# Optimization experiments

Hardware: AMD Instinct MI355X
Metric: run time of the kernel (lower is better)

Reference implementation:

```python
import jax, jax.numpy as jnp
import numpy as np

D_MODEL = 128
K_RED = 3          # fd_redundancy_k
MAX_ITERS = 16     # upper bound on the data-dependent while-loop; masked no-ops after convergence
NEG = -1e9


def setup_inputs() -> dict:
    key = jax.random.key(0)
    ks = jax.random.split(key, 10)
    B, U, S, D, F = 16, 2048, 512, D_MODEL, 32
    return {
        "user_enc": jax.random.normal(ks[0], (B, U, D), jnp.float32),
        "server_enc": jax.random.normal(ks[1], (B, S, D), jnp.float32),
        "users": jax.random.uniform(ks[2], (B, U, 6), jnp.float32),
        "servers": jax.random.uniform(ks[3], (B, S, 7), jnp.float32),
        "connect": jax.random.randint(ks[4], (B, U, S), 0, 2, jnp.int32),
        "fd_onehot": jax.random.randint(ks[5], (B, S, F), 0, 2, jnp.int32),
        "state_proj_w": jax.random.normal(ks[6], (D, 4), jnp.float32) * 0.05,
        "state_proj_b": jnp.zeros((D,), jnp.float32),
        "fd_bias": jnp.asarray(1.0, jnp.float32),
        "ptr_q_w": jax.random.normal(ks[7], (D, D), jnp.float32) * (D ** -0.5),
        "ptr_k_w": jax.random.normal(ks[8], (D, D), jnp.float32) * (D ** -0.5),
        "user_state_w": jax.random.normal(ks[9], (1, 3), jnp.float32) * 0.05,
        "score_bias": jnp.zeros((1,), jnp.float32),
    }


def _forward(user_enc, server_enc, users, servers, connect, fd_onehot,
             state_proj_w, state_proj_b, fd_bias, ptr_q_w, ptr_k_w,
             user_state_w, score_bias):
    B, U, _ = users.shape
    S = servers.shape[1]
    D = user_enc.shape[-1]
    needs = users[..., 2:6]                    # [B,U,4]
    init_cap = servers[..., 3:7]               # [B,S,4]
    connect_mask = connect.astype(bool)
    fd = fd_onehot.astype(jnp.float32)         # [B,S,F] in {0,1}
    F = fd.shape[-1]
    inv_sqrt_d = D ** -0.5
    tk = jnp.float32(max(K_RED, 1))
    q = user_enc @ ptr_q_w.T                   # [B,U,D]  (loop-invariant)
    u_ids = jnp.arange(U)
    s_ids = jnp.arange(S)

    def body(carry, _):
        alloc, cap, seen, logp, flag = carry
        replica_count = alloc.sum(-1)                                    # [B,U]
        need_more = replica_count < K_RED
        can_fulfill = jnp.all(cap[:, None] >= needs[:, :, None], axis=-1)  # [B,U,S]
        eligible = connect_mask & can_fulfill & need_more[..., None] & ~alloc
        go = flag & jnp.any(need_more) & jnp.any(eligible)

        # pointer-attention logits with dynamic server state
        is_new_fd = (jnp.einsum('buf,bsf->bus', seen, fd) < 0.5).astype(jnp.float32)
        cap_ratio = cap / jnp.maximum(init_cap, 1e-6)
        k_vec = (server_enc + cap_ratio @ state_proj_w.T + state_proj_b) @ ptr_k_w.T
        logits = jnp.einsum('bud,bsd->bus', q, k_vec) * inv_sqrt_d + score_bias
        logits = logits + fd_bias * is_new_fd
        rc = replica_count.astype(jnp.float32)
        user_state = jnp.stack([rc / tk,
                                jnp.clip(K_RED - rc, 0.0, None) / tk,
                                (replica_count == K_RED - 1).astype(jnp.float32)], axis=-1)
        logits = logits + user_state @ user_state_w.T                    # broadcast [B,U,1]

        cand = jnp.where(eligible, logits, NEG)
        # each valid server greedily proposes its best eligible user
        valid_server = jnp.any(eligible, axis=1)                         # [B,S]
        prop_u = jnp.argmax(cand, axis=1)                                # [B,S]
        prop_mask = valid_server[:, None, :] & (u_ids[None, :, None] == prop_u[:, None, :])
        logp_prop = jnp.max(cand, axis=1) - jax.nn.logsumexp(cand, axis=1)  # [B,S]

        # each proposed user accepts the highest-scoring proposing server
        acc_cand = jnp.where(prop_mask, logits, NEG)
        has_prop = jnp.any(prop_mask, axis=2)                            # [B,U]
        chosen_s = jnp.argmax(acc_cand, axis=2)                          # [B,U]
        accepted = has_prop[..., None] & (s_ids == chosen_s[..., None])  # [B,U,S]

        alloc = alloc | (accepted & go)
        fd_gain = (jnp.einsum('bus,bsf->buf', prop_mask.astype(jnp.float32), fd) > 0).astype(jnp.float32)
        seen = jnp.where(go, jnp.maximum(seen, fd_gain), seen)
        used = jnp.einsum('bus,buc->bsc', accepted.astype(jnp.float32), needs)
        cap = jnp.where(go, jnp.maximum(cap - used, 0.0), cap)
        gathered = jnp.take_along_axis(logp_prop, chosen_s, axis=1)      # [B,U]
        logp = logp + jnp.where(go & has_prop, gathered, 0.0)
        return (alloc, cap, seen, logp, go), None

    init = (jnp.zeros((B, U, S), bool), init_cap,
            jnp.zeros((B, U, F), jnp.float32), jnp.zeros((B, U), jnp.float32),
            jnp.asarray(True))
    (alloc, cap, seen, logp, _), _ = jax.lax.scan(body, init, None, length=MAX_ITERS)
    return logp.sum(axis=1), alloc, cap


def reference(user_enc, server_enc, users, servers, connect, fd_onehot,
              state_proj_w, state_proj_b, fd_bias, ptr_q_w, ptr_k_w,
              user_state_w, score_bias):
    # policy='greedy' branch of the original forward
    return _forward(user_enc, server_enc, users, servers, connect, fd_onehot,
                    state_proj_w, state_proj_b, fd_bias, ptr_q_w, ptr_k_w,
                    user_state_w, score_bias)
```

## Files before the change

### kernel.cpp

```cpp
#include <hip/hip_runtime.h>
#include <hip/hip_bf16.h>

#define B_N 16
#define U_N 2048
#define S_N 512
#define D_N 128
#define INV_SQRT_D 0.08838834764831845f

typedef unsigned long long ull;
typedef __attribute__((ext_vector_type(8))) short bf16x8;
typedef __attribute__((ext_vector_type(4))) float f32x4;
typedef __attribute__((ext_vector_type(4))) _Float16 f16x4;

__device__ __forceinline__ unsigned monof(float v) {
    unsigned b = __float_as_uint(v);
    return (b & 0x80000000u) ? ~b : (b | 0x80000000u);
}
__device__ __forceinline__ float unmonof(unsigned m) {
    unsigned b = (m & 0x80000000u) ? (m & 0x7fffffffu) : ~m;
    return __uint_as_float(b);
}
__device__ __forceinline__ unsigned short f2bf(float x) {
    unsigned u = __float_as_uint(x);
    return (unsigned short)((u + 0x7fffu + ((u >> 16) & 1u)) >> 16);
}

__global__ void init_pack(const float* __restrict__ servers, const float* __restrict__ users,
                          const int* __restrict__ fd_onehot, const int* __restrict__ connect,
                          ull* __restrict__ connU,
                          unsigned* allocU, uint4* alloc3, unsigned* rcArr, unsigned* seenArr,
                          float* logp, float* capA, float* invA, unsigned* fdm, float* nds,
                          unsigned* any_valid, int* aCnt, int* aList) {
    {
        int r = blockIdx.x * 4 + (threadIdx.x >> 6);
        int lane = threadIdx.x & 63;
        const int* row = connect + (size_t)r * S_N;
        #pragma unroll
        for (int c = 0; c < 8; ++c) {
            ull m = __ballot(row[c * 64 + lane] != 0);
            if (lane == 0) connU[(size_t)r * 8 + c] = m;
        }
    }
    int i = blockIdx.x * 256 + threadIdx.x;
    if (i < B_N * U_N * 16) allocU[i] = 0u;
    if (i < B_N * U_N) {
        rcArr[i] = 0u; seenArr[i] = 0u; logp[i] = 0.f;
        alloc3[i] = make_uint4(0xFFFFFFFFu, 0xFFFFFFFFu, 0xFFFFFFFFu, 0xFFFFFFFFu);
        aList[i] = i & 2047;
        const float* up = users + (size_t)i * 6;
        nds[i * 4 + 0] = up[2]; nds[i * 4 + 1] = up[3];
        nds[i * 4 + 2] = up[4]; nds[i * 4 + 3] = up[5];
    }
    if (i < B_N * S_N) {
        const float* sp = servers + (size_t)i * 7;
        float4 c = make_float4(sp[3], sp[4], sp[5], sp[6]);
        ((float4*)capA)[i] = c;
        ((float4*)invA)[i] = make_float4(1.f / fmaxf(c.x, 1e-6f), 1.f / fmaxf(c.y, 1e-6f),
                                         1.f / fmaxf(c.z, 1e-6f), 1.f / fmaxf(c.w, 1e-6f));
        unsigned w = 0u;
        const int* fp = fd_onehot + (size_t)i * 32;
        #pragma unroll
        for (int f = 0; f < 32; ++f) w |= (fp[f] != 0 ? 1u : 0u) << f;
        fdm[i] = w;
    }
    if (i < 32) aCnt[i] = (i < 16) ? (int)U_N : 0;
    if (i < 16) any_valid[i] = 0u;
}

__global__ __launch_bounds__(256) void gemm_both(const float* __restrict__ user_enc,
                                                 const float* __restrict__ server_enc,
                                                 const float* __restrict__ spb,
                                                 const float* __restrict__ qw,
                                                 const float* __restrict__ kw,
                                                 float* __restrict__ q,
                                                 unsigned short* __restrict__ qb,
                                                 unsigned short* __restrict__ kb) {
    __shared__ float As[16][68];
    __shared__ float Bs[16][68];
    const int z = blockIdx.z;
    const bool isK = blockIdx.x < 8;
    const int xb = isK ? blockIdx.x : blockIdx.x - 8;
    const int M = isK ? S_N : U_N;
    const float* Ab = (isK ? server_enc : user_enc) + (size_t)z * M * D_N;
    const float* Bb = isK ? kw : qw;
    const float scale = isK ? INV_SQRT_D : 1.0f;
    const int m0 = xb * 64, n0 = blockIdx.y * 64;
    const int tid = threadIdx.x;
    const int tx = tid & 15, ty = tid >> 4;
    const int lrow = tid >> 2, lk = (tid & 3) * 4;
    float acc[4][4] = {};
    for (int k0 = 0; k0 < D_N; k0 += 16) {
        float4 av = *(const float4*)(Ab + (size_t)(m0 + lrow) * D_N + k0 + lk);
        float4 bv = *(const float4*)(Bb + (size_t)(n0 + lrow) * D_N + k0 + lk);
        if (isK) {
            const float4 sv = *(const float4*)(spb + k0 + lk);
            av.x += sv.x; av.y += sv.y; av.z += sv.z; av.w += sv.w;
        }
        __syncthreads();
        As[lk + 0][lrow] = av.x; As[lk + 1][lrow] = av.y; As[lk + 2][lrow] = av.z; As[lk + 3][lrow] = av.w;
        Bs[lk + 0][lrow] = bv.x; Bs[lk + 1][lrow] = bv.y; Bs[lk + 2][lrow] = bv.z; Bs[lk + 3][lrow] = bv.w;
        __syncthreads();
        #pragma unroll
        for (int kk = 0; kk < 16; ++kk) {
            float4 a = *(const float4*)&As[kk][ty * 4];
            float4 bq = *(const float4*)&Bs[kk][tx * 4];
            float ar[4] = {a.x, a.y, a.z, a.w}, br[4] = {bq.x, bq.y, bq.z, bq.w};
            #pragma unroll
            for (int ii = 0; ii < 4; ++ii)
                #pragma unroll
                for (int jj = 0; jj < 4; ++jj) acc[ii][jj] += ar[ii] * br[jj];
        }
    }
    #pragma unroll
    for (int ii = 0; ii < 4; ++ii) {
        float4 o = make_float4(acc[ii][0] * scale, acc[ii][1] * scale,
                               acc[ii][2] * scale, acc[ii][3] * scale);
        size_t idx = (size_t)z * M * D_N + (size_t)(m0 + ty * 4 + ii) * D_N + n0 + tx * 4;
        ushort4 ob;
        ob.x = f2bf(o.x); ob.y = f2bf(o.y); ob.z = f2bf(o.z); ob.w = f2bf(o.w);
        if (isK) {
            *(ushort4*)(kb + idx) = ob;
        } else {
            *(float4*)(q + idx) = o;
            *(ushort4*)(qb + idx) = ob;
        }
    }
}

__global__ void qm_kernel(const float* __restrict__ q, const float* __restrict__ kw,
                          const float* __restrict__ spw, float* __restrict__ qm) {
    __shared__ float qs[64][129];
    __shared__ float m2s[512];
    __shared__ float sps[512];
    int b = blockIdx.y, u0 = blockIdx.x * 64;
    int t = threadIdx.x;
    for (int i = t; i < 512; i += 256) sps[i] = spw[i];
    #pragma unroll
    for (int it = 0; it < 8; ++it) {
        int f4 = t + 256 * it;
        int row = f4 >> 5;
        int col = (f4 & 31) * 4;
        float4 v = *(const float4*)(q + ((size_t)(b * U_N + u0 + row)) * D_N + col);
        qs[row][col] = v.x; qs[row][col + 1] = v.y; qs[row][col + 2] = v.z; qs[row][col + 3] = v.w;
    }
    __syncthreads();
    for (int i = t; i < 512; i += 256) {
        int d = i >> 2, c = i & 3;
        float a = 0.f;
        for (int e = 0; e < 128; ++e) a += kw[d * 128 + e] * sps[e * 4 + c];
        m2s[i] = a * INV_SQRT_D;
    }
    __syncthreads();
    int ul = t >> 2, c = t & 3;
    float acc = 0.f;
    for (int d = 0; d < 128; ++d) acc += qs[ul][d] * m2s[d * 4 + c];
    qm[((size_t)(b * U_N + u0 + ul)) * 4 + c] = acc;
}

__global__ __launch_bounds__(256) void qk_mfma(const unsigned short* __restrict__ qb,
                                               const unsigned short* __restrict__ kb,
                                               _Float16* __restrict__ qkh) {
    const int b = blockIdx.z, u0 = blockIdx.x * 128, s0 = blockIdx.y * 64;
    const int t = threadIdx.x, w = t >> 6, l = t & 63;
    const int lr = l & 15, lq = l >> 4;
    const unsigned short* Ab = qb + ((size_t)(b * U_N + u0 + w * 32 + lr)) * D_N + lq * 8;
    const unsigned short* Bb = kb + ((size_t)(b * S_N + s0 + lr)) * D_N + lq * 8;
    f32x4 acc[2][4] = {};
    #pragma unroll
    for (int kt = 0; kt < 4; ++kt) {
        bf16x8 a0 = *(const bf16x8*)(Ab + kt * 32);
        bf16x8 a1 = *(const bf16x8*)(Ab + 16 * D_N + kt * 32);
        #pragma unroll
        for (int c = 0; c < 4; ++c) {
            bf16x8 bf = *(const bf16x8*)(Bb + c * 16 * D_N + kt * 32);
            acc[0][c] = __builtin_amdgcn_mfma_f32_16x16x32_bf16(a0, bf, acc[0][c], 0, 0, 0);
            acc[1][c] = __builtin_amdgcn_mfma_f32_16x16x32_bf16(a1, bf, acc[1][c], 0, 0, 0);
        }
    }
    __shared__ _Float16 Cs[128][72];
    #pragma unroll
    for (int mt = 0; mt < 2; ++mt)
        #pragma unroll
        for (int c = 0; c < 4; ++c)
            #pragma unroll
            for (int r = 0; r < 4; ++r)
                Cs[w * 32 + mt * 16 + lq * 4 + r][c * 16 + lr] = (_Float16)acc[mt][c][r];
    __syncthreads();
    #pragma unroll
    for (int k = 0; k < 4; ++k) {
        int row = (t >> 3) + k * 32;
        int sg = (t & 7) * 8;
        uint4 v = *(const uint4*)&Cs[row][sg];
        *(uint4*)(qkh + ((size_t)(b * U_N + u0 + row)) * S_N + s0 + sg) = v;
    }
}

__global__ __launch_bounds__(256) void iter_score(
    const _Float16* __restrict__ qkh, const float* __restrict__ qm4,
    const float* __restrict__ nds, const unsigned* __restrict__ connU32,
    const uint4* __restrict__ alloc3, const unsigned* __restrict__ rcArr,
    const unsigned* __restrict__ seenArr, const unsigned* __restrict__ fdm_,
    const float* __restrict__ capA, const float* __restrict__ invA,
    const float* __restrict__ usw, const float* __restrict__ sbp, const float* __restrict__ fdbp,
    ull* __restrict__ keypart, float* __restrict__ sumpart,
    const unsigned* __restrict__ any_valid, const int* __restrict__ aCnt,
    const int* __restrict__ aList, int iter) {
    if (iter > 0 && any_valid[iter - 1] == 0u) return;
    const int tid = threadIdx.x;
    const int b = blockIdx.x & 15;
    const int ublk = blockIdx.x >> 4;
    const int p = iter & 1;
    const int cnt = aCnt[p * 16 + b];
    const int u0 = ublk << 5;
    if (u0 >= cnt) return;
    const int h = tid >> 7;
    const int sl = tid & 127;
    const int s0 = sl * 4;
    const float w0 = usw[0], w1 = usw[1], w2 = usw[2], sb = sbp[0], fdb = fdbp[0];
    const float ub0 = sb + w1;
    const float ub1 = sb + w0 * (1.f / 3.f) + w1 * (2.f / 3.f);
    const float ub2 = sb + w0 * (2.f / 3.f) + w1 * (1.f / 3.f) + w2;
    const int bsb = b * S_N + s0;
    float4 cap[4], cr[4]; unsigned fq[4];
    #pragma unroll
    for (int j = 0; j < 4; ++j) {
        cap[j] = ((const float4*)capA)[bsb + j];
        float4 iv = ((const float4*)invA)[bsb + j];
        cr[j] = make_float4(cap[j].x * iv.x, cap[j].y * iv.y, cap[j].z * iv.z, cap[j].w * iv.w);
        fq[j] = fdm_[bsb + j];
    }
    ull k[4] = {0ULL, 0ULL, 0ULL, 0ULL};
    float e[4] = {0.f, 0.f, 0.f, 0.f};
    const int nloc = cnt - (u0 + h * 16);
    const int4* lp = (const int4*)(aList + p * (B_N * U_N) + b * U_N + u0 + h * 16);
    const int nsh = (sl & 7) * 4;
    #pragma unroll 1
    for (int c4 = 0; c4 < 4; ++c4) {
        const int nrem = nloc - c4 * 4;
        if (nrem <= 0) break;
        const int4 L = lp[c4];
        #pragma unroll
        for (int x = 0; x < 4; ++x) {
            if (x < nrem) {
                const int ulid = (&L.x)[x];
                const int gu = b * U_N + ulid;
                const unsigned rcu = rcArr[gu];
                const f16x4 qv = *(const f16x4*)(qkh + (size_t)gu * S_N + s0);
                const float4 qmv = ((const float4*)qm4)[gu];
                const float4 ndv = ((const float4*)nds)[gu];
                const unsigned snu = seenArr[gu];
                const uint4 al = alloc3[gu];
                const unsigned nib = connU32[gu * 16 + (sl >> 3)] >> nsh;
                const float add = (rcu == 0u) ? ub0 : ((rcu == 1u) ? ub1 : ub2);
                const unsigned uinv = ~(unsigned)ulid;
                #pragma unroll
                for (int j = 0; j < 4; ++j) {
                    const unsigned us = (unsigned)(s0 + j);
                    const bool ful = (cap[j].x >= ndv.x) & (cap[j].y >= ndv.y) &
                                     (cap[j].z >= ndv.z) & (cap[j].w >= ndv.w);
                    const bool aok = (al.x != us) & (al.y != us) & (al.z != us);
                    const bool el = (((nib >> j) & 1u) != 0u) & ful & aok;
                    const float lg = (float)qv[j] + qmv.x * cr[j].x + qmv.y * cr[j].y +
                                     qmv.z * cr[j].z + qmv.w * cr[j].w + add +
                                     (((snu & fq[j]) == 0u) ? fdb : 0.f);
                    if (el) {
                        const ull kk = ((ull)monof(lg) << 32) | uinv;
                        k[j] = k[j] > kk ? k[j] : kk;
                        e[j] += __expf(lg);
                    }
                }
            }
        }
    }
    __shared__ ull mk[128][4];
    __shared__ float me[128][4];
    if (h == 1) {
        #pragma unroll
        for (int j = 0; j < 4; ++j) { mk[sl][j] = k[j]; me[sl][j] = e[j]; }
    }
    __syncthreads();
    if (h == 0) {
        #pragma unroll
        for (int j = 0; j < 4; ++j) {
            const ull o = mk[sl][j];
            k[j] = o > k[j] ? o : k[j];
            e[j] += me[sl][j];
        }
        const size_t pp = (size_t)ublk * (B_N * S_N) + bsb;
        ulonglong2 ka; ka.x = k[0]; ka.y = k[1];
        ulonglong2 kc; kc.x = k[2]; kc.y = k[3];
        *(ulonglong2*)(keypart + pp) = ka;
        *(ulonglong2*)(keypart + pp + 2) = kc;
        *(float4*)(sumpart + pp) = make_float4(e[0], e[1], e[2], e[3]);
    }
}

__global__ __launch_bounds__(1024) void iter_midapply(
    const ull* __restrict__ keypart, const float* __restrict__ sumpart,
    const unsigned* __restrict__ fdm_, const float* __restrict__ nds,
    uint4* __restrict__ alloc3, unsigned* __restrict__ allocU,
    unsigned* __restrict__ rcArr, unsigned* __restrict__ seenArr,
    float* __restrict__ capA, float* __restrict__ logp,
    unsigned* __restrict__ any_valid, int* __restrict__ aCnt,
    int* __restrict__ aList, int iter) {
    if (iter > 0 && any_valid[iter - 1] == 0u) return;
    __shared__ ull ukeyL[2048];
    __shared__ unsigned sgL[2048];
    __shared__ ull bkL[512];
    __shared__ float bsL[512];
    __shared__ float lpL[512];
    __shared__ unsigned propF;
    const int b = blockIdx.x, t = threadIdx.x;
    const int p = iter & 1, np = 1 - p;
    const int cnt = aCnt[p * 16 + b];
    if (t == 0) { aCnt[np * 16 + b] = 0; propF = 0u; }
    ukeyL[t] = 0ULL; ukeyL[t + 1024] = 0ULL;
    sgL[t] = 0u; sgL[t + 1024] = 0u;
    __syncthreads();
    const int nblk = (cnt + 31) >> 5;
    const int jmid = nblk >> 1;
    const int s = t & 511, h = t >> 9;
    const int base = b * S_N + s;
    ull best = 0ULL; float ssum = 0.f;
    const int j0 = h == 0 ? 0 : jmid;
    const int j1 = h == 0 ? jmid : nblk;
    #pragma unroll 4
    for (int j = j0; j < j1; ++j) {
        const ull kk = keypart[(size_t)j * (B_N * S_N) + base];
        best = kk > best ? kk : best;
        ssum += sumpart[(size_t)j * (B_N * S_N) + base];
    }
    if (h == 0) { bkL[s] = best; bsL[s] = ssum; }
    __syncthreads();
    if (h == 1) {
        const ull ob = bkL[s];
        best = ob > best ? ob : best;
        ssum += bsL[s];
        if (best != 0ULL) {
            const float mx = unmonof((unsigned)(best >> 32));
            const unsigned pu = ~(unsigned)best;
            lpL[s] = mx - __logf(ssum);
            atomicMax(&ukeyL[pu], ((ull)monof(mx) << 32) | (~(unsigned)s));
            atomicOr(&sgL[pu], fdm_[base]);
            atomicOr(&propF, 1u);
        }
    }
    __syncthreads();
    if (t == 0 && propF != 0u) atomicOr(&any_valid[iter], 1u);
    #pragma unroll
    for (int g = 0; g < 2; ++g) {
        const int u = t + g * 1024;
        const int gu = b * U_N + u;
        const ull key = ukeyL[u];
        unsigned r = rcArr[gu];
        if (key != 0ULL) {
            const unsigned s2 = ~(unsigned)key;
            const int bs2 = b * S_N + (int)s2;
            uint4 al = alloc3[gu];
            if (r == 0u) al.x = s2; else if (r == 1u) al.y = s2; else al.z = s2;
            alloc3[gu] = al;
            allocU[gu * 16 + (s2 >> 5)] |= 1u << (s2 & 31u);
            const float4 nd = ((const float4*)nds)[gu];
            float4 cv = ((float4*)capA)[bs2];
            cv.x = fmaxf(cv.x - nd.x, 0.f); cv.y = fmaxf(cv.y - nd.y, 0.f);
            cv.z = fmaxf(cv.z - nd.z, 0.f); cv.w = fmaxf(cv.w - nd.w, 0.f);
            ((float4*)capA)[bs2] = cv;
            r += 1u;
            rcArr[gu] = r;
            logp[gu] += lpL[s2];
            seenArr[gu] |= sgL[u];
        }
        const bool act = r < 3u;
        const ull bal = __ballot(act);
        const int lane = t & 63;
        int wbase = 0;
        if (lane == 0 && bal != 0ULL)
            wbase = atomicAdd(&aCnt[np * 16 + b], (int)__popcll(bal));
        wbase = __shfl(wbase, 0, 64);
        if (act)
            aList[np * (B_N * U_N) + b * U_N + wbase +
                  (int)__popcll(bal & ((1ULL << lane) - 1ULL))] = u;
    }
}

__global__ void finalize_all(const unsigned* __restrict__ allocU, const float* __restrict__ capA,
                             const float* __restrict__ logp, float* __restrict__ out) {
    const int bid = blockIdx.x, t = threadIdx.x;
    const int idx = bid * 256 + t;
    {
        const int bu = idx >> 7;
        const int s4 = (idx & 127) * 4;
        const unsigned w = allocU[bu * 16 + (s4 >> 5)];
        float4 o;
        o.x = ((w >> ((s4 + 0) & 31)) & 1u) ? 1.f : 0.f;
        o.y = ((w >> ((s4 + 1) & 31)) & 1u) ? 1.f : 0.f;
        o.z = ((w >> ((s4 + 2) & 31)) & 1u) ? 1.f : 0.f;
        o.w = ((w >> ((s4 + 3) & 31)) & 1u) ? 1.f : 0.f;
        *(float4*)(out + 16 + (size_t)bu * S_N + s4) = o;
    }
    if (idx < B_N * S_N * 4) out[16 + (size_t)B_N * U_N * S_N + idx] = capA[idx];
    if (bid >= 16368) {
        const int b = bid - 16368;
        float s = 0.f;
        for (int u = t; u < U_N; u += 256) s += logp[b * U_N + u];
        #pragma unroll
        for (int m = 1; m < 64; m <<= 1) s += __shfl_xor(s, m, 64);
        __shared__ float r[4];
        if ((t & 63) == 0) r[t >> 6] = s;
        __syncthreads();
        if (t == 0) out[b] = r[0] + r[1] + r[2] + r[3];
    }
}

extern "C" void kernel_launch(void* const* d_in, const int* in_sizes, int n_in,
                              void* d_out, int out_size, void* d_ws, size_t ws_size,
                              hipStream_t stream) {
    const float* user_enc = (const float*)d_in[0];
    const float* server_enc = (const float*)d_in[1];
    const float* users = (const float*)d_in[2];
    const float* servers = (const float*)d_in[3];
    const int* connect = (const int*)d_in[4];
    const int* fd_onehot = (const int*)d_in[5];
    const float* state_proj_w = (const float*)d_in[6];
    const float* state_proj_b = (const float*)d_in[7];
    const float* fd_bias = (const float*)d_in[8];
    const float* ptr_q_w = (const float*)d_in[9];
    const float* ptr_k_w = (const float*)d_in[10];
    const float* user_state_w = (const float*)d_in[11];
    const float* score_bias = (const float*)d_in[12];
    float* out = (float*)d_out;

    char* w = (char*)d_ws;
    _Float16* qkh = (_Float16*)(w + 0);
    float* q = (float*)(w + 33554432);
    unsigned short* qb = (unsigned short*)(w + 50331648);
    unsigned short* kb = (unsigned short*)(w + 58720256);
    ull* keypart = (ull*)(w + 60817408);
    float* sumpart = (float*)(w + 65011712);
    float* qm = (float*)(w + 67108864);
    ull* connU = (ull*)(w + 67633152);
    unsigned* allocU = (unsigned*)(w + 69730304);
    uint4* alloc3 = (uint4*)(w + 71827456);
    float* nds = (float*)(w + 72351744);
    unsigned* fdm = (unsigned*)(w + 72876032);
    float* capA = (float*)(w + 72908800);
    float* invA = (float*)(w + 73039872);
    unsigned* rcArr = (unsigned*)(w + 73170944);
    unsigned* seenArr = (unsigned*)(w + 73302016);
    float* logp = (float*)(w + 73433088);
    unsigned* any_valid = (unsigned*)(w + 73564160);
    int* aCnt = (int*)(w + 73564288);
    int* aList = (int*)(w + 73564416);

    init_pack<<<8192, 256, 0, stream>>>(servers, users, fd_onehot, connect, connU,
                                        allocU, alloc3, rcArr, seenArr, logp, capA, invA,
                                        fdm, nds, any_valid, aCnt, aList);
    gemm_both<<<dim3(40, 2, 16), 256, 0, stream>>>(user_enc, server_enc, state_proj_b,
                                                   ptr_q_w, ptr_k_w, q, qb, kb);
    qm_kernel<<<dim3(32, 16), 256, 0, stream>>>(q, ptr_k_w, state_proj_w, qm);
    qk_mfma<<<dim3(16, 8, 16), 256, 0, stream>>>(qb, kb, qkh);
    for (int it = 0; it < 16; ++it) {
        iter_score<<<1024, 256, 0, stream>>>(qkh, qm, nds, (const unsigned*)connU, alloc3, rcArr,
                                             seenArr, fdm, capA, invA, user_state_w, score_bias,
                                             fd_bias, keypart, sumpart, any_valid, aCnt, aList, it);
        iter_midapply<<<16, 1024, 0, stream>>>(keypart, sumpart, fdm, nds, alloc3, allocU,
                                               rcArr, seenArr, capA, logp, any_valid,
                                               aCnt, aList, it);
    }
    finalize_all<<<16384, 256, 0, stream>>>(allocU, capA, logp, out);
}
```

Measured before the change: 501.0 us.

## Fuse per-iteration score and apply kernels via last-block-done atomic counter

```diff
diff --git a/kernel.cpp b/kernel.cpp
--- a/kernel.cpp
+++ b/kernel.cpp
@@ -6,6 +6,7 @@
 #define S_N 512
 #define D_N 128
 #define INV_SQRT_D 0.08838834764831845f
+#define BPB 64
 
 typedef unsigned long long ull;
 typedef __attribute__((ext_vector_type(8))) short bf16x8;
@@ -30,7 +31,7 @@
                           ull* __restrict__ connU,
                           unsigned* allocU, uint4* alloc3, unsigned* rcArr, unsigned* seenArr,
                           float* logp, float* capA, float* invA, unsigned* fdm, float* nds,
-                          unsigned* any_valid, int* aCnt, int* aList) {
+                          unsigned* any_valid, int* aCnt, int* aList, unsigned* done_cnt) {
     {
         int r = blockIdx.x * 4 + (threadIdx.x >> 6);
         int lane = threadIdx.x & 63;
@@ -63,6 +64,7 @@
         for (int f = 0; f < 32; ++f) w |= (fp[f] != 0 ? 1u : 0u) << f;
         fdm[i] = w;
     }
+    if (i < 256) done_cnt[i] = 0u;
     if (i < 32) aCnt[i] = (i < 16) ? (int)U_N : 0;
     if (i < 16) any_valid[i] = 0u;
 }
@@ -195,184 +197,187 @@
     }
 }
 
-__global__ __launch_bounds__(256) void iter_score(
+__global__ __launch_bounds__(256) void iter_fused(
     const _Float16* __restrict__ qkh, const float* __restrict__ qm4,
     const float* __restrict__ nds, const unsigned* __restrict__ connU32,
-    const uint4* __restrict__ alloc3, const unsigned* __restrict__ rcArr,
-    const unsigned* __restrict__ seenArr, const unsigned* __restrict__ fdm_,
-    const float* __restrict__ capA, const float* __restrict__ invA,
+    uint4* __restrict__ alloc3, unsigned* __restrict__ rcArr,
+    unsigned* __restrict__ seenArr, const unsigned* __restrict__ fdm_,
+    float* __restrict__ capA, const float* __restrict__ invA,
     const float* __restrict__ usw, const float* __restrict__ sbp, const float* __restrict__ fdbp,
     ull* __restrict__ keypart, float* __restrict__ sumpart,
-    const unsigned* __restrict__ any_valid, const int* __restrict__ aCnt,
-    const int* __restrict__ aList, int iter) {
+    unsigned* __restrict__ allocU, float* __restrict__ logp,
+    unsigned* __restrict__ any_valid, unsigned* __restrict__ done_cnt,
+    unsigned* __restrict__ eligMask, int* __restrict__ aCnt,
+    int* __restrict__ aList, int iter) {
     if (iter > 0 && any_valid[iter - 1] == 0u) return;
     const int tid = threadIdx.x;
     const int b = blockIdx.x & 15;
     const int ublk = blockIdx.x >> 4;
-    const int p = iter & 1;
+    const int p = iter & 1, np = 1 - p;
     const int cnt = aCnt[p * 16 + b];
     const int u0 = ublk << 5;
-    if (u0 >= cnt) return;
-    const int h = tid >> 7;
-    const int sl = tid & 127;
-    const int s0 = sl * 4;
-    const float w0 = usw[0], w1 = usw[1], w2 = usw[2], sb = sbp[0], fdb = fdbp[0];
-    const float ub0 = sb + w1;
-    const float ub1 = sb + w0 * (1.f / 3.f) + w1 * (2.f / 3.f);
-    const float ub2 = sb + w0 * (2.f / 3.f) + w1 * (1.f / 3.f) + w2;
-    const int bsb = b * S_N + s0;
-    float4 cap[4], cr[4]; unsigned fq[4];
-    #pragma unroll
-    for (int j = 0; j < 4; ++j) {
-        cap[j] = ((const float4*)capA)[bsb + j];
-        float4 iv = ((const float4*)invA)[bsb + j];
-        cr[j] = make_float4(cap[j].x * iv.x, cap[j].y * iv.y, cap[j].z * iv.z, cap[j].w * iv.w);
-        fq[j] = fdm_[bsb + j];
-    }
-    ull k[4] = {0ULL, 0ULL, 0ULL, 0ULL};
-    float e[4] = {0.f, 0.f, 0.f, 0.f};
-    const int nloc = cnt - (u0 + h * 16);
-    const int4* lp = (const int4*)(aList + p * (B_N * U_N) + b * U_N + u0 + h * 16);
-    const int nsh = (sl & 7) * 4;
-    #pragma unroll 1
-    for (int c4 = 0; c4 < 4; ++c4) {
-        const int nrem = nloc - c4 * 4;
-        if (nrem <= 0) break;
-        const int4 L = lp[c4];
-        #pragma unroll
-        for (int x = 0; x < 4; ++x) {
-            if (x < nrem) {
-                const int ulid = (&L.x)[x];
-                const int gu = b * U_N + ulid;
-                const unsigned rcu = rcArr[gu];
-                const f16x4 qv = *(const f16x4*)(qkh + (size_t)gu * S_N + s0);
-                const float4 qmv = ((const float4*)qm4)[gu];
-                const float4 ndv = ((const float4*)nds)[gu];
-                const unsigned snu = seenArr[gu];
-                const uint4 al = alloc3[gu];
-                const unsigned nib = connU32[gu * 16 + (sl >> 3)] >> nsh;
-                const float add = (rcu == 0u) ? ub0 : ((rcu == 1u) ? ub1 : ub2);
-                const unsigned uinv = ~(unsigned)ulid;
-                #pragma unroll
-                for (int j = 0; j < 4; ++j) {
-                    const unsigned us = (unsigned)(s0 + j);
-                    const bool ful = (cap[j].x >= ndv.x) & (cap[j].y >= ndv.y) &
-                                     (cap[j].z >= ndv.z) & (cap[j].w >= ndv.w);
-                    const bool aok = (al.x != us) & (al.y != us) & (al.z != us);
-                    const bool el = (((nib >> j) & 1u) != 0u) & ful & aok;
-                    const float lg = (float)qv[j] + qmv.x * cr[j].x + qmv.y * cr[j].y +
-                                     qmv.z * cr[j].z + qmv.w * cr[j].w + add +
-                                     (((snu & fq[j]) == 0u) ? fdb : 0.f);
-                    if (el) {
-                        const ull kk = ((ull)monof(lg) << 32) | uinv;
-                        k[j] = k[j] > kk ? k[j] : kk;
-                        e[j] += __expf(lg);
+    __shared__ ull mk[128][4];
+    __shared__ float me[128][4];
+    __shared__ unsigned emL[4];
+    __shared__ ull ukeyL[2048];
+    __shared__ unsigned sgL[2048];
+    __shared__ float lpL[512];
+    __shared__ unsigned propF, lastF;
+    if (u0 < cnt) {
+        const int h = tid >> 7;
+        const int sl = tid & 127;
+        const int s0 = sl * 4;
+        const float w0 = usw[0], w1 = usw[1], w2 = usw[2], sb = sbp[0], fdb = fdbp[0];
+        const float ub0 = sb + w1;
+        const float ub1 = sb + w0 * (1.f / 3.f) + w1 * (2.f / 3.f);
+        const float ub2 = sb + w0 * (2.f / 3.f) + w1 * (1.f / 3.f) + w2;
+        const int bsb = b * S_N + s0;
+        float4 cap[4], cr[4]; unsigned fq[4];
+        #pragma unroll
+        for (int j = 0; j < 4; ++j) {
+            cap[j] = ((const float4*)capA)[bsb + j];
+            float4 iv = ((const float4*)invA)[bsb + j];
+            cr[j] = make_float4(cap[j].x * iv.x, cap[j].y * iv.y, cap[j].z * iv.z, cap[j].w * iv.w);
+            fq[j] = fdm_[bsb + j];
+        }
+        ull k[4] = {0ULL, 0ULL, 0ULL, 0ULL};
+        float e[4] = {0.f, 0.f, 0.f, 0.f};
+        unsigned elm = 0u;
+        const int nloc = cnt - (u0 + h * 16);
+        const int4* lp = (const int4*)(aList + p * (B_N * U_N) + b * U_N + u0 + h * 16);
+        const int nsh = (sl & 7) * 4;
+        #pragma unroll 1
+        for (int c4 = 0; c4 < 4; ++c4) {
+            const int nrem = nloc - c4 * 4;
+            if (nrem <= 0) break;
+            const int4 L = lp[c4];
+            #pragma unroll
+            for (int x = 0; x < 4; ++x) {
+                if (x < nrem) {
+                    const int ulid = (&L.x)[x];
+                    const int gu = b * U_N + ulid;
+                    const unsigned rcu = rcArr[gu];
+                    const f16x4 qv = *(const f16x4*)(qkh + (size_t)gu * S_N + s0);
+                    const float4 qmv = ((const float4*)qm4)[gu];
+                    const float4 ndv = ((const float4*)nds)[gu];
+                    const unsigned snu = seenArr[gu];
+                    const uint4 al = alloc3[gu];
+                    const unsigned nib = connU32[gu * 16 + (sl >> 3)] >> nsh;
+                    const float add = (rcu == 0u) ? ub0 : ((rcu == 1u) ? ub1 : ub2);
+                    const unsigned uinv = ~(unsigned)ulid;
+                    #pragma unroll
+                    for (int j = 0; j < 4; ++j) {
+                        const unsigned us = (unsigned)(s0 + j);
+                        const bool ful = (cap[j].x >= ndv.x) & (cap[j].y >= ndv.y) &
+                                         (cap[j].z >= ndv.z) & (cap[j].w >= ndv.w);
+                        const bool aok = (al.x != us) & (al.y != us) & (al.z != us);
+                        const bool el = (((nib >> j) & 1u) != 0u) & ful & aok;
+                        const float lg = (float)qv[j] + qmv.x * cr[j].x + qmv.y * cr[j].y +
+                                         qmv.z * cr[j].z + qmv.w * cr[j].w + add +
+                                         (((snu & fq[j]) == 0u) ? fdb : 0.f);
+                        if (el) {
+                            elm |= 1u << (c4 * 4 + x);
+                            const ull kk = ((ull)monof(lg) << 32) | uinv;
+                            k[j] = k[j] > kk ? k[j] : kk;
+                            e[j] += __expf(lg);
+                        }
                     }
                 }
             }
         }
-    }
-    __shared__ ull mk[128][4];
-    __shared__ float me[128][4];
-    if (h == 1) {
-        #pragma unroll
-        for (int j = 0; j < 4; ++j) { mk[sl][j] = k[j]; me[sl][j] = e[j]; }
-    }
-    __syncthreads();
-    if (h == 0) {
-        #pragma unroll
-        for (int j = 0; j < 4; ++j) {
-            const ull o = mk[sl][j];
-            k[j] = o > k[j] ? o : k[j];
-            e[j] += me[sl][j];
-        }
-        const size_t pp = (size_t)ublk * (B_N * S_N) + bsb;
-        ulonglong2 ka; ka.x = k[0]; ka.y = k[1];
-        ulonglong2 kc; kc.x = k[2]; kc.y = k[3];
-        *(ulonglong2*)(keypart + pp) = ka;
-        *(ulonglong2*)(keypart + pp + 2) = kc;
-        *(float4*)(sumpart + pp) = make_float4(e[0], e[1], e[2], e[3]);
-    }
-}
-
-__global__ __launch_bounds__(1024) void iter_midapply(
-    const ull* __restrict__ keypart, const float* __restrict__ sumpart,
-    const unsigned* __restrict__ fdm_, const float* __restrict__ nds,
-    uint4* __restrict__ alloc3, unsigned* __restrict__ allocU,
-    unsigned* __restrict__ rcArr, unsigned* __restrict__ seenArr,
-    float* __restrict__ capA, float* __restrict__ logp,
-    unsigned* __restrict__ any_valid, int* __restrict__ aCnt,
-    int* __restrict__ aList, int iter) {
-    if (iter > 0 && any_valid[iter - 1] == 0u) return;
-    __shared__ ull ukeyL[2048];
-    __shared__ unsigned sgL[2048];
-    __shared__ ull bkL[512];
-    __shared__ float bsL[512];
-    __shared__ float lpL[512];
-    __shared__ unsigned propF;
-    const int b = blockIdx.x, t = threadIdx.x;
-    const int p = iter & 1, np = 1 - p;
-    const int cnt = aCnt[p * 16 + b];
-    if (t == 0) { aCnt[np * 16 + b] = 0; propF = 0u; }
-    ukeyL[t] = 0ULL; ukeyL[t + 1024] = 0ULL;
-    sgL[t] = 0u; sgL[t + 1024] = 0u;
-    __syncthreads();
+        #pragma unroll
+        for (int m = 1; m < 64; m <<= 1) elm |= __shfl_xor(elm, m, 64);
+        if ((tid & 63) == 0) emL[tid >> 6] = elm;
+        if (h == 1) {
+            #pragma unroll
+            for (int j = 0; j < 4; ++j) { mk[sl][j] = k[j]; me[sl][j] = e[j]; }
+        }
+        __syncthreads();
+        if (h == 0) {
+            #pragma unroll
+            for (int j = 0; j < 4; ++j) {
+                const ull o = mk[sl][j];
+                k[j] = o > k[j] ? o : k[j];
+                e[j] += me[sl][j];
+            }
+            const size_t pp = (size_t)ublk * (B_N * S_N) + bsb;
+            ulonglong2 ka; ka.x = k[0]; ka.y = k[1];
+            ulonglong2 kc; kc.x = k[2]; kc.y = k[3];
+            *(ulonglong2*)(keypart + pp) = ka;
+            *(ulonglong2*)(keypart + pp + 2) = kc;
+            *(float4*)(sumpart + pp) = make_float4(e[0], e[1], e[2], e[3]);
+        }
+        if (tid == 0)
+            eligMask[ublk * 16 + b] = (emL[0] | emL[1]) | ((emL[2] | emL[3]) << 16);
+    }
+    #pragma unroll
+    for (int g = 0; g < 8; ++g) { ukeyL[tid + g * 256] = 0ULL; sgL[tid + g * 256] = 0u; }
+    if (tid == 0) propF = 0u;
+    __syncthreads();
+    if (tid == 0) {
+        __threadfence();
+        lastF = (atomicAdd(&done_cnt[iter * 16 + b], 1u) == (unsigned)(BPB - 1)) ? 1u : 0u;
+    }
+    __syncthreads();
+    if (!lastF) return;
+    __threadfence();
     const int nblk = (cnt + 31) >> 5;
-    const int jmid = nblk >> 1;
-    const int s = t & 511, h = t >> 9;
-    const int base = b * S_N + s;
-    ull best = 0ULL; float ssum = 0.f;
-    const int j0 = h == 0 ? 0 : jmid;
-    const int j1 = h == 0 ? jmid : nblk;
-    #pragma unroll 4
-    for (int j = j0; j < j1; ++j) {
-        const ull kk = keypart[(size_t)j * (B_N * S_N) + base];
-        best = kk > best ? kk : best;
-        ssum += sumpart[(size_t)j * (B_N * S_N) + base];
-    }
-    if (h == 0) { bkL[s] = best; bsL[s] = ssum; }
-    __syncthreads();
-    if (h == 1) {
-        const ull ob = bkL[s];
-        best = ob > best ? ob : best;
-        ssum += bsL[s];
+    #pragma unroll
+    for (int half = 0; half < 2; ++half) {
+        const int s = tid + half * 256;
+        const int base = b * S_N + s;
+        ull best = 0ULL; float ssum = 0.f;
+        #pragma unroll 4
+        for (int j = 0; j < nblk; ++j) {
+            const ull kk = keypart[(size_t)j * (B_N * S_N) + base];
+            best = kk > best ? kk : best;
+            ssum += sumpart[(size_t)j * (B_N * S_N) + base];
+        }
         if (best != 0ULL) {
             const float mx = unmonof((unsigned)(best >> 32));
             const unsigned pu = ~(unsigned)best;
             lpL[s] = mx - __logf(ssum);
             atomicMax(&ukeyL[pu], ((ull)monof(mx) << 32) | (~(unsigned)s));
             atomicOr(&sgL[pu], fdm_[base]);
-            atomicOr(&propF, 1u);
-        }
-    }
-    __syncthreads();
-    if (t == 0 && propF != 0u) atomicOr(&any_valid[iter], 1u);
-    #pragma unroll
-    for (int g = 0; g < 2; ++g) {
-        const int u = t + g * 1024;
-        const int gu = b * U_N + u;
-        const ull key = ukeyL[u];
-        unsigned r = rcArr[gu];
-        if (key != 0ULL) {
-            const unsigned s2 = ~(unsigned)key;
-            const int bs2 = b * S_N + (int)s2;
-            uint4 al = alloc3[gu];
-            if (r == 0u) al.x = s2; else if (r == 1u) al.y = s2; else al.z = s2;
-            alloc3[gu] = al;
-            allocU[gu * 16 + (s2 >> 5)] |= 1u << (s2 & 31u);
-            const float4 nd = ((const float4*)nds)[gu];
-            float4 cv = ((float4*)capA)[bs2];
-            cv.x = fmaxf(cv.x - nd.x, 0.f); cv.y = fmaxf(cv.y - nd.y, 0.f);
-            cv.z = fmaxf(cv.z - nd.z, 0.f); cv.w = fmaxf(cv.w - nd.w, 0.f);
-            ((float4*)capA)[bs2] = cv;
-            r += 1u;
-            rcArr[gu] = r;
-            logp[gu] += lpL[s2];
-            seenArr[gu] |= sgL[u];
-        }
-        const bool act = r < 3u;
+            propF = 1u;
+        }
+    }
+    __syncthreads();
+    if (tid == 0) {
+        if (propF != 0u) any_valid[iter] = 1u;
+        aCnt[np * 16 + b] = 0;
+    }
+    __syncthreads();
+    for (int i0 = 0; i0 < cnt; i0 += 256) {
+        const int i = i0 + tid;
+        int u = 0; bool act = false;
+        if (i < cnt) {
+            u = aList[p * (B_N * U_N) + b * U_N + i];
+            const int gu = b * U_N + u;
+            unsigned r = rcArr[gu];
+            const ull key = ukeyL[u];
+            if (key != 0ULL) {
+                const unsigned s2 = ~(unsigned)key;
+                const int bs2 = b * S_N + (int)s2;
+                uint4 al = alloc3[gu];
+                if (r == 0u) al.x = s2; else if (r == 1u) al.y = s2; else al.z = s2;
+                alloc3[gu] = al;
+                allocU[gu * 16 + (s2 >> 5)] |= 1u << (s2 & 31u);
+                const float4 nd = ((const float4*)nds)[gu];
+                float4 cv = ((float4*)capA)[bs2];
+                cv.x = fmaxf(cv.x - nd.x, 0.f); cv.y = fmaxf(cv.y - nd.y, 0.f);
+                cv.z = fmaxf(cv.z - nd.z, 0.f); cv.w = fmaxf(cv.w - nd.w, 0.f);
+                ((float4*)capA)[bs2] = cv;
+                r += 1u;
+                rcArr[gu] = r;
+                logp[gu] += lpL[(int)s2];
+                seenArr[gu] |= sgL[u];
+            }
+            const unsigned em = eligMask[(i >> 5) * 16 + b];
+            act = (r < 3u) && (((em >> (i & 31)) & 1u) != 0u);
+        }
         const ull bal = __ballot(act);
-        const int lane = t & 63;
+        const int lane = tid & 63;
         int wbase = 0;
         if (lane == 0 && bal != 0ULL)
             wbase = atomicAdd(&aCnt[np * 16 + b], (int)__popcll(bal));
@@ -450,22 +455,22 @@
     float* logp = (float*)(w + 73433088);
     unsigned* any_valid = (unsigned*)(w + 73564160);
     int* aCnt = (int*)(w + 73564288);
-    int* aList = (int*)(w + 73564416);
+    unsigned* done_cnt = (unsigned*)(w + 73564416);
+    unsigned* eligMask = (unsigned*)(w + 73565440);
+    int* aList = (int*)(w + 73569536);
 
     init_pack<<<8192, 256, 0, stream>>>(servers, users, fd_onehot, connect, connU,
                                         allocU, alloc3, rcArr, seenArr, logp, capA, invA,
-                                        fdm, nds, any_valid, aCnt, aList);
+                                        fdm, nds, any_valid, aCnt, aList, done_cnt);
     gemm_both<<<dim3(40, 2, 16), 256, 0, stream>>>(user_enc, server_enc, state_proj_b,
                                                    ptr_q_w, ptr_k_w, q, qb, kb);
     qm_kernel<<<dim3(32, 16), 256, 0, stream>>>(q, ptr_k_w, state_proj_w, qm);
     qk_mfma<<<dim3(16, 8, 16), 256, 0, stream>>>(qb, kb, qkh);
     for (int it = 0; it < 16; ++it) {
-        iter_score<<<1024, 256, 0, stream>>>(qkh, qm, nds, (const unsigned*)connU, alloc3, rcArr,
+        iter_fused<<<1024, 256, 0, stream>>>(qkh, qm, nds, (const unsigned*)connU, alloc3, rcArr,
                                              seenArr, fdm, capA, invA, user_state_w, score_bias,
-                                             fd_bias, keypart, sumpart, any_valid, aCnt, aList, it);
-        iter_midapply<<<16, 1024, 0, stream>>>(keypart, sumpart, fdm, nds, alloc3, allocU,
-                                               rcArr, seenArr, capA, logp, any_valid,
-                                               aCnt, aList, it);
+                                             fd_bias, keypart, sumpart, allocU, logp,
+                                             any_valid, done_cnt, eligMask, aCnt, aList, it);
     }
     finalize_all<<<16384, 256, 0, stream>>>(allocU, capA, logp, out);
 }
```

Measured after the change: 568.1 us. +13.4%, slower.
